# Performance work log

Measured on AMD Instinct MI355X. Metric: run time of the kernel, lower is better.

The kernel has to match this reference:

```python
import math
import jax, jax.numpy as jnp
import numpy as np

B, C, H, W = 32, 256, 32, 32  # in==mid==out channels

def setup_inputs() -> dict:
    key = jax.random.key(0)
    ks = jax.random.split(key, 3)
    x = jax.random.normal(ks[0], (B, C, H, W), dtype=jnp.float32)
    # 1x1 convs are just channel matmuls: weight [out_ch, in_ch]
    w_in = jax.random.normal(ks[1], (3 * C, C), dtype=jnp.float32) * (1.0 / math.sqrt(C))
    b_in = jnp.zeros((3 * C,), dtype=jnp.float32)
    # project_out has init_scale=0.0 in the original; we use random weights so the
    # output (and gradients) are non-trivial, but the math is identical.
    w_out = jax.random.normal(ks[2], (C, C), dtype=jnp.float32) * (1.0 / math.sqrt(C))
    b_out = jnp.zeros((C,), dtype=jnp.float32)
    return {"x": x, "w_in": w_in, "b_in": b_in, "w_out": w_out, "b_out": b_out}

def _qkv_attention(q, k, v):
    # q,k,v: [B,C,H,W]. Full spatial self-attention over the HxW grid.
    b, c, h, w = q.shape
    scores = jnp.einsum('bchw,bcHW->bhwHW', q, k)          # [B,H,W,H,W]
    scores = scores.reshape(b, h, w, h * w) / math.sqrt(c)
    attn = jax.nn.softmax(scores, axis=-1).reshape(b, h, w, h, w)
    return jnp.einsum('bhwHW,bcHW->bchw', attn, v)          # [B,C,H,W]

def reference(x, w_in, b_in, w_out, b_out):
    skip = x  # in_channels == out_channels -> Identity skip
    qkv = jnp.einsum('oc,bchw->bohw', w_in, x) + b_in[None, :, None, None]
    q, k, v = jnp.split(qkv, 3, axis=1)
    h = _qkv_attention(q, k, v)
    out = jnp.einsum('oc,bchw->bohw', w_out, h) + b_out[None, :, None, None]
    return out + skip
```

## Files before the change

### kernel.cpp

```cpp
#include <hip/hip_runtime.h>
#include <hip/hip_bf16.h>

typedef __attribute__((ext_vector_type(8))) short bf16x8;
typedef __attribute__((ext_vector_type(4))) float f32x4;
typedef __attribute__((ext_vector_type(16))) float f32x16;
typedef long long i64;

#define NB 32
#define NC 256
#define NN 1024

__device__ __forceinline__ unsigned pack2(float a, float b) {
    __hip_bfloat16 ha = __float2bfloat16(a), hb = __float2bfloat16(b);
    unsigned short ua = *(unsigned short*)&ha, ub = *(unsigned short*)&hb;
    return (unsigned)ua | ((unsigned)ub << 16);
}

__device__ __forceinline__ float bflo(unsigned u) {
    union { unsigned i; float f; } x; x.i = u << 16; return x.f;
}
__device__ __forceinline__ float bfhi(unsigned u) {
    union { unsigned i; float f; } x; x.i = u & 0xffff0000u; return x.f;
}
__device__ __forceinline__ unsigned fp8x4(float a, float b, float c, float d) {
    int w = __builtin_amdgcn_cvt_pk_fp8_f32(a, b, 0, false);
    w = __builtin_amdgcn_cvt_pk_fp8_f32(c, d, w, true);
    return (unsigned)w;
}

__device__ __forceinline__ void glds16(const void* g, void* lds) {
    __builtin_amdgcn_global_load_lds(
        (const __attribute__((address_space(1))) unsigned int*)g,
        (__attribute__((address_space(3))) unsigned int*)lds, 16, 0, 0);
}

__global__ __launch_bounds__(256) void xpose_kernel(
    const float* __restrict__ x, unsigned char* __restrict__ Xt8)
{
    __shared__ float Ls[64 * 67];
    const int t = threadIdx.x;
    const int n0 = blockIdx.x * 64, c0 = blockIdx.y * 64, b = blockIdx.z;
    const int cl = t >> 4, nl = (t & 15) * 4;
    const float* xb = x + ((size_t)b * NC + c0) * NN + n0;
    #pragma unroll
    for (int q4 = 0; q4 < 4; ++q4) {
        const int c = cl + q4 * 16;
        const float4 v = *(const float4*)(xb + (size_t)c * NN + nl);
        Ls[(nl + 0) * 67 + c] = v.x;
        Ls[(nl + 1) * 67 + c] = v.y;
        Ls[(nl + 2) * 67 + c] = v.z;
        Ls[(nl + 3) * 67 + c] = v.w;
    }
    __syncthreads();
    #pragma unroll
    for (int p = 0; p < 2; ++p) {
        const int idx = p * 256 + t, n = idx >> 3, cs = idx & 7;
        const float* r = &Ls[n * 67 + cs * 8];
        uint2 o;
        o.x = fp8x4(r[0], r[1], r[2], r[3]);
        o.y = fp8x4(r[4], r[5], r[6], r[7]);
        *(uint2*)(Xt8 + ((size_t)b * NN + n0 + n) * 256 + c0 + cs * 8) = o;
    }
}

__device__ __forceinline__ void stage_ab8(const unsigned char* __restrict__ Ag,
                                          const float* __restrict__ Bg,
                                          char* Ad, char* Bd, int ks, int t)
{
    #pragma unroll
    for (int p = 0; p < 2; ++p) {
        const int idx = p * 256 + t;
        const int row = idx >> 2, pc = idx & 3;
        const int lp = pc ^ (row & 3);
        glds16(Ag + (size_t)row * 256 + ks * 64 + lp * 16, Ad + idx * 16);
        const float* wp = Bg + (size_t)row * NC + ks * 64 + lp * 16;
        const float4 u0 = *(const float4*)wp;
        const float4 u1 = *(const float4*)(wp + 4);
        const float4 u2 = *(const float4*)(wp + 8);
        const float4 u3 = *(const float4*)(wp + 12);
        uint4 pk;
        pk.x = fp8x4(u0.x, u0.y, u0.z, u0.w);
        pk.y = fp8x4(u1.x, u1.y, u1.z, u1.w);
        pk.z = fp8x4(u2.x, u2.y, u2.z, u2.w);
        pk.w = fp8x4(u3.x, u3.y, u3.z, u3.w);
        *(uint4*)(Bd + idx * 16) = pk;
    }
}

__global__ __launch_bounds__(256, 3) void qkv_gemm_kernel(
    const unsigned char* __restrict__ Xt8, const float* __restrict__ w_in,
    const float* __restrict__ b_in, unsigned char* __restrict__ Qt8,
    unsigned char* __restrict__ Kt8, unsigned char* __restrict__ Vf8)
{
    __shared__ char smem[34816];
    char* const A0 = smem;
    char* const A1 = smem + 8192;
    char* const B0 = smem + 16384;
    char* const B1 = smem + 24576;

    const int t  = threadIdx.x;
    const int wv = t >> 6, ln = t & 63, lo = ln & 15, hi = ln >> 4;
    const int wm = wv >> 1, wn = wv & 1;
    const int n0 = blockIdx.x * 128, o0 = blockIdx.y * 128, b = blockIdx.z;

    const unsigned char* Ag = Xt8 + ((size_t)b * NN + n0) * 256;
    const float* Bg = w_in + (size_t)o0 * NC;

    f32x4 acc[4][4];
    #pragma unroll
    for (int i = 0; i < 4; ++i)
        #pragma unroll
        for (int j = 0; j < 4; ++j) acc[i][j] = (f32x4){0.f, 0.f, 0.f, 0.f};

    int ra[4], rb[4];
    #pragma unroll
    for (int f = 0; f < 4; ++f) { ra[f] = wm * 64 + f * 16 + lo; rb[f] = wn * 64 + f * 16 + lo; }

    stage_ab8(Ag, Bg, A0, B0, 0, t);
    __syncthreads();
    #pragma unroll
    for (int ks = 0; ks < 4; ++ks) {
        char* Ac = (ks & 1) ? A1 : A0;
        char* Bc = (ks & 1) ? B1 : B0;
        if (ks < 3)
            stage_ab8(Ag, Bg, (ks & 1) ? A0 : A1, (ks & 1) ? B0 : B1, ks + 1, t);
        #pragma unroll
        for (int kk = 0; kk < 2; ++kk) {
            i64 av[4], bv[4];
            #pragma unroll
            for (int f = 0; f < 4; ++f) {
                av[f] = *(const i64*)(Ac + ra[f] * 64 + (((kk << 2) | hi) ^ ((ra[f] & 3) << 1)) * 8);
                bv[f] = *(const i64*)(Bc + rb[f] * 64 + (((kk << 2) | hi) ^ ((rb[f] & 3) << 1)) * 8);
            }
            #pragma unroll
            for (int fm = 0; fm < 4; ++fm)
                #pragma unroll
                for (int fn = 0; fn < 4; ++fn)
                    acc[fm][fn] = __builtin_amdgcn_mfma_f32_16x16x32_fp8_fp8(
                        av[fm], bv[fn], acc[fm][fn], 0, 0, 0);
        }
        __syncthreads();
    }

    float bias[4];
    #pragma unroll
    for (int fn = 0; fn < 4; ++fn) bias[fn] = b_in[o0 + wn * 64 + fn * 16 + lo];

    __hip_bfloat16* Ls = (__hip_bfloat16*)smem;
    if (o0 < 512) {
        #pragma unroll
        for (int fm = 0; fm < 4; ++fm)
            #pragma unroll
            for (int fn = 0; fn < 4; ++fn)
                #pragma unroll
                for (int r = 0; r < 4; ++r)
                    Ls[(wm * 64 + fm * 16 + hi * 4 + r) * 136 + wn * 64 + fn * 16 + lo] =
                        __float2bfloat16(acc[fm][fn][r] + bias[fn]);
        __syncthreads();
        unsigned char* dst = (o0 < 256) ? Qt8 : Kt8;
        const int oc = (o0 < 256) ? o0 : o0 - 256;
        #pragma unroll
        for (int p = 0; p < 4; ++p) {
            const int idx = p * 256 + t, row = idx >> 3, ch = idx & 7;
            const unsigned* ls = (const unsigned*)&Ls[row * 136 + ch * 16];
            const uint4 a = *(const uint4*)ls;
            const uint4 b2 = *(const uint4*)(ls + 4);
            uint4 o;
            o.x = fp8x4(bflo(a.x), bfhi(a.x), bflo(a.y), bfhi(a.y));
            o.y = fp8x4(bflo(a.z), bfhi(a.z), bflo(a.w), bfhi(a.w));
            o.z = fp8x4(bflo(b2.x), bfhi(b2.x), bflo(b2.y), bfhi(b2.y));
            o.w = fp8x4(bflo(b2.z), bfhi(b2.z), bflo(b2.w), bfhi(b2.w));
            *(uint4*)(dst + ((size_t)b * NN + n0 + row) * 256 + oc + ch * 16) = o;
        }
    } else {
        #pragma unroll
        for (int fm = 0; fm < 4; ++fm)
            #pragma unroll
            for (int fn = 0; fn < 4; ++fn)
                #pragma unroll
                for (int r = 0; r < 4; ++r)
                    Ls[(wn * 64 + fn * 16 + lo) * 136 + wm * 64 + fm * 16 + hi * 4 + r] =
                        __float2bfloat16(acc[fm][fn][r] + bias[fn]);
        __syncthreads();
        #pragma unroll
        for (int p = 0; p < 8; ++p) {
            const int idx = p * 256 + t;
            const int ch = idx >> 7, cr = idx & 127;
            const unsigned* ls = (const unsigned*)&Ls[cr * 136 + ch * 8];
            const uint4 a = *(const uint4*)ls;
            uint2 o;
            o.x = fp8x4(bflo(a.x), bfhi(a.x), bflo(a.y), bfhi(a.y));
            o.y = fp8x4(bflo(a.z), bfhi(a.z), bflo(a.w), bfhi(a.w));
            const int g = (n0 >> 3) + ch;
            *(uint2*)(Vf8 + (((size_t)b * 128 + g) * 256 + (o0 - 512) + cr) * 8) = o;
        }
    }
}

__device__ __forceinline__ void stage_tile(const unsigned char* __restrict__ Kb,
                                           const unsigned char* __restrict__ Vb,
                                           char* Kd, char* Vd, int m0, int t)
{
    {
        const int row = t >> 4, pc = t & 15;
        const int prow = (row & 19) | ((row & 4) << 1) | ((row & 8) >> 1);
        const int sc = pc ^ (row & 15);
        glds16(Kb + (size_t)(m0 + prow) * 256 + sc * 16, Kd + t * 16);
    }
    {
        glds16(Vb + (size_t)(m0 >> 3) * 2048 + t * 16, Vd + t * 16);
    }
}

__global__ __launch_bounds__(512, 2) void attn_kernel(
    const unsigned char* __restrict__ Qt8, const unsigned char* __restrict__ Kt8,
    const unsigned char* __restrict__ Vf8, const float* __restrict__ w_out,
    const float* __restrict__ b_out, const float* __restrict__ xg,
    float* __restrict__ out)
{
    __shared__ char smem[139264];

    const int t  = threadIdx.x;
    const int wv = t >> 6, ln = t & 63;
    const int l32 = ln & 31, h2 = ln >> 5;
    const int qgrp = wv & 3, half = wv >> 2;
    const int wid = blockIdx.x + 8 * blockIdx.y;
    const int swz = (wid & 7) * 32 + (wid >> 3);
    const int qb = swz & 7, b = swz >> 3;
    const int n0 = qb * 128;
    const float scale = 0.0625f;

    const unsigned char* Kbase = Kt8 + (size_t)b * NN * 256;
    const unsigned char* Vbase = Vf8 + (size_t)b * 128 * 2048;

    const unsigned char* qp = Qt8 + ((size_t)b * NN + n0 + qgrp * 32 + l32) * 256;
    i64 qf[16];
    #pragma unroll
    for (int ks = 0; ks < 16; ++ks)
        qf[ks] = *(const i64*)(qp + ks * 16 + h2 * 8);

    f32x16 acc[8];
    #pragma unroll
    for (int ct = 0; ct < 8; ++ct)
        #pragma unroll
        for (int r = 0; r < 16; ++r) acc[ct][r] = 0.f;
    float mr = 0.f;
    float sr = 0.f;

    #pragma unroll
    for (int tt = 0; tt < 4; ++tt)
        stage_tile(Kbase, Vbase, smem + (tt & 3) * 8192,
                   smem + 32768 + (tt & 7) * 8192, tt * 32, t);
    __syncthreads();

    i64 pb_prev[2];
    pb_prev[0] = 0; pb_prev[1] = 0;
    const char* Vc_prev = smem + 32768;

    for (int s = 0; s < 16; ++s) {
        if (s < 15) {
            const int t2 = 2 * s + 2, t3 = 2 * s + 3;
            stage_tile(Kbase, Vbase, smem + (t2 & 3) * 8192,
                       smem + 32768 + (t2 & 7) * 8192, t2 * 32, t);
            stage_tile(Kbase, Vbase, smem + (t3 & 3) * 8192,
                       smem + 32768 + (t3 & 7) * 8192, t3 * 32, t);
        }
        const int tile = 2 * s + half;
        char* const Kc = smem + (tile & 3) * 8192;
        char* const Vc = smem + 32768 + (tile & 7) * 8192;

        f32x16 sfA, sfB;
        #pragma unroll
        for (int r = 0; r < 16; ++r) { sfA[r] = 0.f; sfB[r] = 0.f; }
        __builtin_amdgcn_s_setprio(1);
        #pragma unroll
        for (int ks = 0; ks < 8; ++ks) {
            const int pc = ks ^ (l32 & 15);
            const i64 kf = *(const i64*)(Kc + l32 * 256 + pc * 16 + h2 * 8);
            sfA = __builtin_amdgcn_mfma_f32_32x32x16_fp8_fp8(kf, qf[ks], sfA, 0, 0, 0);
        }
        #pragma unroll
        for (int ks = 8; ks < 16; ++ks) {
            const int pc = ks ^ (l32 & 15);
            const i64 kf = *(const i64*)(Kc + l32 * 256 + pc * 16 + h2 * 8);
            sfB = __builtin_amdgcn_mfma_f32_32x32x16_fp8_fp8(kf, qf[ks], sfB, 0, 0, 0);
        }

        if (s > 0) {
            #pragma unroll
            for (int ct = 0; ct < 8; ++ct) {
                #pragma unroll
                for (int kstep = 0; kstep < 2; ++kstep) {
                    const i64 vf = *(const i64*)(Vc_prev + (2 * kstep + h2) * 2048 +
                                                 (ct * 32 + l32) * 8);
                    acc[ct] = __builtin_amdgcn_mfma_f32_32x32x16_fp8_fp8(vf, pb_prev[kstep], acc[ct], 0, 0, 0);
                }
            }
        }
        __builtin_amdgcn_s_setprio(0);

        float sv[16];
        #pragma unroll
        for (int r = 0; r < 16; ++r) sv[r] = sfA[r] + sfB[r];

        float m0a = fmaxf(sv[0], sv[1]),  m1a = fmaxf(sv[2], sv[3]);
        float m2a = fmaxf(sv[4], sv[5]),  m3a = fmaxf(sv[6], sv[7]);
        float m4a = fmaxf(sv[8], sv[9]),  m5a = fmaxf(sv[10], sv[11]);
        float m6a = fmaxf(sv[12], sv[13]), m7a = fmaxf(sv[14], sv[15]);
        float m0b = fmaxf(m0a, m1a), m1b = fmaxf(m2a, m3a);
        float m2b = fmaxf(m4a, m5a), m3b = fmaxf(m6a, m7a);
        float tm = fmaxf(fmaxf(m0b, m1b), fmaxf(m2b, m3b));
        tm = fmaxf(tm, __shfl_xor(tm, 32, 64));
        tm *= scale;
        if (__any(tm > mr + 8.f)) {
            const float mn = fmaxf(mr, tm);
            const float al = __expf(mr - mn);
            mr = mn;
            sr *= al;
            #pragma unroll
            for (int ct = 0; ct < 8; ++ct)
                #pragma unroll
                for (int r = 0; r < 16; ++r) acc[ct][r] *= al;
        }
        float p[16];
        #pragma unroll
        for (int r = 0; r < 16; ++r)
            p[r] = __expf(sv[r] * scale - mr);
        float s0a = p[0] + p[1],  s1a = p[2] + p[3];
        float s2a = p[4] + p[5],  s3a = p[6] + p[7];
        float s4a = p[8] + p[9],  s5a = p[10] + p[11];
        float s6a = p[12] + p[13], s7a = p[14] + p[15];
        float sacc = ((s0a + s1a) + (s2a + s3a)) + ((s4a + s5a) + (s6a + s7a));
        sacc += __shfl_xor(sacc, 32, 64);
        sr += sacc;

        #pragma unroll
        for (int kstep = 0; kstep < 2; ++kstep) {
            union { unsigned u[2]; i64 l; } uu;
            uu.u[0] = fp8x4(p[8 * kstep + 0], p[8 * kstep + 1],
                            p[8 * kstep + 2], p[8 * kstep + 3]);
            uu.u[1] = fp8x4(p[8 * kstep + 4], p[8 * kstep + 5],
                            p[8 * kstep + 6], p[8 * kstep + 7]);
            pb_prev[kstep] = uu.l;
        }
        Vc_prev = Vc;
        __syncthreads();
    }

    __builtin_amdgcn_s_setprio(1);
    #pragma unroll
    for (int ct = 0; ct < 8; ++ct) {
        #pragma unroll
        for (int kstep = 0; kstep < 2; ++kstep) {
            const i64 vf = *(const i64*)(Vc_prev + (2 * kstep + h2) * 2048 +
                                         (ct * 32 + l32) * 8);
            acc[ct] = __builtin_amdgcn_mfma_f32_32x32x16_fp8_fp8(vf, pb_prev[kstep], acc[ct], 0, 0, 0);
        }
    }
    __builtin_amdgcn_s_setprio(0);

    float* const ex = (float*)smem;
    __hip_bfloat16* const Hld = (__hip_bfloat16*)(smem + 69632);
    #pragma unroll
    for (int ph = 0; ph < 2; ++ph) {
        if (half == 1 && (qgrp >> 1) == ph) {
            float* dst = ex + ((qgrp & 1) * 64 + ln) * 132;
            #pragma unroll
            for (int ct = 0; ct < 8; ++ct)
                #pragma unroll
                for (int rr = 0; rr < 4; ++rr) {
                    f32x4 v = {acc[ct][rr * 4 + 0], acc[ct][rr * 4 + 1],
                               acc[ct][rr * 4 + 2], acc[ct][rr * 4 + 3]};
                    *(f32x4*)(dst + ct * 16 + rr * 4) = v;
                }
            dst[128] = mr;
            dst[129] = sr;
        }
        __syncthreads();
        if (half == 0 && (qgrp >> 1) == ph) {
            const float* src = ex + ((qgrp & 1) * 64 + ln) * 132;
            const float mb = src[128], lb = src[129];
            const float m = fmaxf(mr, mb);
            float fa = __expf(mr - m), fb = __expf(mb - m);
            const float inv = 1.0f / (sr * fa + lb * fb);
            fa *= inv; fb *= inv;
            __hip_bfloat16* hrow = Hld + (size_t)(qgrp * 32 + l32) * 264;
            #pragma unroll
            for (int ct = 0; ct < 8; ++ct)
                #pragma unroll
                for (int ss = 0; ss < 4; ++ss) {
                    const float o0 = acc[ct][ss * 4 + 0] * fa + src[ct * 16 + ss * 4 + 0] * fb;
                    const float o1 = acc[ct][ss * 4 + 1] * fa + src[ct * 16 + ss * 4 + 1] * fb;
                    const float o2 = acc[ct][ss * 4 + 2] * fa + src[ct * 16 + ss * 4 + 2] * fb;
                    const float o3 = acc[ct][ss * 4 + 3] * fa + src[ct * 16 + ss * 4 + 3] * fb;
                    uint2 v;
                    v.x = pack2(o0, o1);
                    v.y = pack2(o2, o3);
                    *(uint2*)(hrow + ct * 32 + ss * 8 + h2 * 4) = v;
                }
        }
        __syncthreads();
    }

    __hip_bfloat16* const Wld = (__hip_bfloat16*)smem;
    const int oT = wv >> 1;
    const int nT0 = (wv & 1) * 2, nT1 = nT0 + 1;
    for (int oh = 0; oh < 2; ++oh) {
        #pragma unroll
        for (int p = 0; p < 8; ++p) {
            const int idx = p * 512 + t;
            const int o = idx >> 5, ck = idx & 31;
            const float* wp = w_out + (size_t)(oh * 128 + o) * NC + ck * 8;
            const float4 u0 = *(const float4*)wp;
            const float4 u1 = *(const float4*)(wp + 4);
            uint4 pk;
            pk.x = pack2(u0.x, u0.y); pk.y = pack2(u0.z, u0.w);
            pk.z = pack2(u1.x, u1.y); pk.w = pack2(u1.z, u1.w);
            *(uint4*)((char*)Wld + (size_t)o * 528 + ck * 16) = pk;
        }
        __syncthreads();

        f32x16 oc0, oc1;
        #pragma unroll
        for (int r = 0; r < 16; ++r) { oc0[r] = 0.f; oc1[r] = 0.f; }
        __builtin_amdgcn_s_setprio(1);
        #pragma unroll
        for (int ks = 0; ks < 16; ++ks) {
            const int ck = ks * 2 + h2;
            bf16x8 wf = *(const bf16x8*)((char*)Wld + (size_t)(oT * 32 + l32) * 528 + ck * 16);
            bf16x8 hf0 = *(const bf16x8*)((char*)Hld + (size_t)(nT0 * 32 + l32) * 528 + ck * 16);
            bf16x8 hf1 = *(const bf16x8*)((char*)Hld + (size_t)(nT1 * 32 + l32) * 528 + ck * 16);
            oc0 = __builtin_amdgcn_mfma_f32_32x32x16_bf16(wf, hf0, oc0, 0, 0, 0);
            oc1 = __builtin_amdgcn_mfma_f32_32x32x16_bf16(wf, hf1, oc1, 0, 0, 0);
        }
        __builtin_amdgcn_s_setprio(0);

        #pragma unroll
        for (int r = 0; r < 16; ++r) {
            const int o = oh * 128 + oT * 32 + (r & 3) + 8 * (r >> 2) + 4 * h2;
            const float bo = b_out[o];
            const size_t rowg = ((size_t)b * NC + o) * NN + n0;
            const size_t g0 = rowg + nT0 * 32 + l32;
            const size_t g1 = rowg + nT1 * 32 + l32;
            out[g0] = oc0[r] + bo + xg[g0];
            out[g1] = oc1[r] + bo + xg[g1];
        }
        __syncthreads();
    }
}

extern "C" void kernel_launch(void* const* d_in, const int* in_sizes, int n_in,
                              void* d_out, int out_size, void* d_ws, size_t ws_size,
                              hipStream_t stream) {
    const float* x     = (const float*)d_in[0];
    const float* w_in  = (const float*)d_in[1];
    const float* b_in  = (const float*)d_in[2];
    const float* w_out = (const float*)d_in[3];
    const float* b_out = (const float*)d_in[4];
    float* out = (float*)d_out;

    if (ws_size < (size_t)32 * 1024 * 1024) return;
    char* ws = (char*)d_ws;
    unsigned char* Qt8 = (unsigned char*)(ws);
    unsigned char* Kt8 = (unsigned char*)(ws + ((size_t)8 << 20));
    unsigned char* Vf8 = (unsigned char*)(ws + ((size_t)16 << 20));
    unsigned char* Xt8 = (unsigned char*)(ws + ((size_t)24 << 20));

    xpose_kernel<<<dim3(16, 4, 32), 256, 0, stream>>>(x, Xt8);
    qkv_gemm_kernel<<<dim3(8, 6, 32), 256, 0, stream>>>(Xt8, w_in, b_in, Qt8, Kt8, Vf8);
    attn_kernel<<<dim3(8, 32), 512, 0, stream>>>(Qt8, Kt8, Vf8, w_out, b_out, x, out);
}
```

Measured before the change: 85.86 us.

## Deepen K/V LDS ring to 8 tiles with vmcnt waits, drop PV software pipelining

```diff
diff --git a/kernel.cpp b/kernel.cpp
--- a/kernel.cpp
+++ b/kernel.cpp
@@ -249,25 +249,26 @@
 
     #pragma unroll
     for (int tt = 0; tt < 4; ++tt)
-        stage_tile(Kbase, Vbase, smem + (tt & 3) * 8192,
-                   smem + 32768 + (tt & 7) * 8192, tt * 32, t);
-    __syncthreads();
-
-    i64 pb_prev[2];
-    pb_prev[0] = 0; pb_prev[1] = 0;
-    const char* Vc_prev = smem + 32768;
+        stage_tile(Kbase, Vbase, smem + tt * 8192,
+                   smem + 65536 + tt * 8192, tt * 32, t);
 
     for (int s = 0; s < 16; ++s) {
-        if (s < 15) {
-            const int t2 = 2 * s + 2, t3 = 2 * s + 3;
-            stage_tile(Kbase, Vbase, smem + (t2 & 3) * 8192,
-                       smem + 32768 + (t2 & 7) * 8192, t2 * 32, t);
-            stage_tile(Kbase, Vbase, smem + (t3 & 3) * 8192,
-                       smem + 32768 + (t3 & 7) * 8192, t3 * 32, t);
-        }
+        if (s < 14) {
+            const int t2 = 2 * s + 4, t3 = 2 * s + 5;
+            stage_tile(Kbase, Vbase, smem + (t2 & 7) * 8192,
+                       smem + 65536 + (t2 & 7) * 8192, t2 * 32, t);
+            stage_tile(Kbase, Vbase, smem + (t3 & 7) * 8192,
+                       smem + 65536 + (t3 & 7) * 8192, t3 * 32, t);
+        }
+        if (s <= 13)      asm volatile("s_waitcnt vmcnt(8)" ::: "memory");
+        else if (s == 14) asm volatile("s_waitcnt vmcnt(4)" ::: "memory");
+        else              asm volatile("s_waitcnt vmcnt(0)" ::: "memory");
+        __builtin_amdgcn_s_barrier();
+        __builtin_amdgcn_sched_barrier(0);
+
         const int tile = 2 * s + half;
-        char* const Kc = smem + (tile & 3) * 8192;
-        char* const Vc = smem + 32768 + (tile & 7) * 8192;
+        char* const Kc = smem + (tile & 7) * 8192;
+        char* const Vc = smem + 65536 + (tile & 7) * 8192;
 
         f32x16 sfA, sfB;
         #pragma unroll
@@ -284,18 +285,6 @@
             const int pc = ks ^ (l32 & 15);
             const i64 kf = *(const i64*)(Kc + l32 * 256 + pc * 16 + h2 * 8);
             sfB = __builtin_amdgcn_mfma_f32_32x32x16_fp8_fp8(kf, qf[ks], sfB, 0, 0, 0);
-        }
-
-        if (s > 0) {
-            #pragma unroll
-            for (int ct = 0; ct < 8; ++ct) {
-                #pragma unroll
-                for (int kstep = 0; kstep < 2; ++kstep) {
-                    const i64 vf = *(const i64*)(Vc_prev + (2 * kstep + h2) * 2048 +
-                                                 (ct * 32 + l32) * 8);
-                    acc[ct] = __builtin_amdgcn_mfma_f32_32x32x16_fp8_fp8(vf, pb_prev[kstep], acc[ct], 0, 0, 0);
-                }
-            }
         }
         __builtin_amdgcn_s_setprio(0);
 
@@ -334,6 +323,7 @@
         sacc += __shfl_xor(sacc, 32, 64);
         sr += sacc;
 
+        i64 pb[2];
         #pragma unroll
         for (int kstep = 0; kstep < 2; ++kstep) {
             union { unsigned u[2]; i64 l; } uu;
@@ -341,23 +331,22 @@
                             p[8 * kstep + 2], p[8 * kstep + 3]);
             uu.u[1] = fp8x4(p[8 * kstep + 4], p[8 * kstep + 5],
                             p[8 * kstep + 6], p[8 * kstep + 7]);
-            pb_prev[kstep] = uu.l;
-        }
-        Vc_prev = Vc;
-        __syncthreads();
-    }
-
-    __builtin_amdgcn_s_setprio(1);
-    #pragma unroll
-    for (int ct = 0; ct < 8; ++ct) {
-        #pragma unroll
-        for (int kstep = 0; kstep < 2; ++kstep) {
-            const i64 vf = *(const i64*)(Vc_prev + (2 * kstep + h2) * 2048 +
-                                         (ct * 32 + l32) * 8);
-            acc[ct] = __builtin_amdgcn_mfma_f32_32x32x16_fp8_fp8(vf, pb_prev[kstep], acc[ct], 0, 0, 0);
-        }
-    }
-    __builtin_amdgcn_s_setprio(0);
+            pb[kstep] = uu.l;
+        }
+
+        __builtin_amdgcn_s_setprio(1);
+        #pragma unroll
+        for (int ct = 0; ct < 8; ++ct) {
+            #pragma unroll
+            for (int kstep = 0; kstep < 2; ++kstep) {
+                const i64 vf = *(const i64*)(Vc + (2 * kstep + h2) * 2048 +
+                                             (ct * 32 + l32) * 8);
+                acc[ct] = __builtin_amdgcn_mfma_f32_32x32x16_fp8_fp8(vf, pb[kstep], acc[ct], 0, 0, 0);
+            }
+        }
+        __builtin_amdgcn_s_setprio(0);
+    }
+    __syncthreads();
 
     float* const ex = (float*)smem;
     __hip_bfloat16* const Hld = (__hip_bfloat16*)(smem + 69632);
```

Result: no change. 85.16 us (-0.8%).
